# Optimization experiments

Hardware: AMD Instinct MI355X
Metric: run time of the kernel (lower is better)

The kernel has to match this reference:

```python
import jax, jax.numpy as jnp
import numpy as np

B, N, K, D_MODEL = 4, 16384, 32, 64

def gather_neighbors(x, idx):
    # x: [B, N, F], idx: [B, N, K] -> [B, N, K, F]
    return jnp.take_along_axis(x[:, :, None, :], idx[:, :, :, None], axis=1)

def setup_inputs() -> dict:
    key = jax.random.key(0)
    k1, k2, k3, k4, k5 = jax.random.split(key, 5)
    x = jax.random.normal(k1, (B, N, D_MODEL), dtype=jnp.float32)
    pos = jax.random.normal(k2, (B, N, 3), dtype=jnp.float32)
    neighbor_idx = jax.random.randint(k3, (B, N, K), 0, N, dtype=jnp.int32)
    W1 = jax.random.normal(k4, (3, D_MODEL), dtype=jnp.float32) * (1.0 / np.sqrt(3.0))
    b1 = jnp.zeros((D_MODEL,), dtype=jnp.float32)
    W2 = jax.random.normal(k5, (D_MODEL, D_MODEL), dtype=jnp.float32) * (1.0 / np.sqrt(D_MODEL))
    b2 = jnp.zeros((D_MODEL,), dtype=jnp.float32)
    return {"x": x, "pos": pos, "neighbor_idx": neighbor_idx,
            "W1": W1, "b1": b1, "W2": W2, "b2": b2}

def reference(x, pos, neighbor_idx, W1, b1, W2, b2):
    # gather neighbor positions: [B, N, K, 3]
    neighbors = gather_neighbors(pos, neighbor_idx)
    rel_pos = pos[:, :, None, :] - neighbors              # [B, N, K, 3]
    # weight MLP: Linear(3,d) + LeakyReLU(0.1), Linear(d,d)
    h = jax.nn.leaky_relu(jnp.einsum('bnkd,df->bnkf', rel_pos, W1) + b1, 0.1)
    w = jnp.einsum('bnkf,fg->bnkg', h, W2) + b2           # [B, N, K, F]
    xg = gather_neighbors(x, neighbor_idx)                # [B, N, K, F]
    return jnp.sum(w * xg, axis=2)                        # [B, N, F]
```

## Files before the change

### kernel.cpp

```cpp
#include <hip/hip_runtime.h>


#define NPTS   16384
#define KNB    32
#define F      64
#define BATCH  4
#define LOG2N  14
#define WPTS   8

typedef _Float16 h2     __attribute__((ext_vector_type(2)));
typedef _Float16 h8     __attribute__((ext_vector_type(8)));
typedef float    f32x16 __attribute__((ext_vector_type(16)));

__global__ __launch_bounds__(256, 2) void pointconv_mfma(
    const float* __restrict__ x,
    const float* __restrict__ pos,
    const int*   __restrict__ idx,
    const float* __restrict__ W1,
    const float* __restrict__ b1,
    const float* __restrict__ W2,
    const float* __restrict__ b2,
    float*       __restrict__ out)
{
    __shared__ __align__(16) _Float16 w1p[32][8];
    __shared__ __align__(16) _Float16 w2f[2][4][2][32][8];

    const int tid = threadIdx.x;
    if (tid < 32) {
        const int g = 2 * tid;
        w1p[tid][0] = (_Float16)W1[0 * F + g]; w1p[tid][1] = (_Float16)W1[0 * F + g + 1];
        w1p[tid][2] = (_Float16)W1[1 * F + g]; w1p[tid][3] = (_Float16)W1[1 * F + g + 1];
        w1p[tid][4] = (_Float16)W1[2 * F + g]; w1p[tid][5] = (_Float16)W1[2 * F + g + 1];
        w1p[tid][6] = (_Float16)b1[g];         w1p[tid][7] = (_Float16)b1[g + 1];
    }
#pragma unroll
    for (int r = 0; r < 16; ++r) {
        const int e = r * 256 + tid;
        const int g = e >> 6, f = e & 63;
        w2f[(g >> 3) & 1][g >> 4][f & 1][f >> 1][g & 7] = (_Float16)W2[e];
    }
    __syncthreads();

    const int lane = tid & 63;
    const int wv   = tid >> 6;
    const int m    = lane & 31;
    const int hf   = lane >> 5;

    h8 bfrag[4][2];
#pragma unroll
    for (int t = 0; t < 4; ++t)
#pragma unroll
        for (int c = 0; c < 2; ++c)
            bfrag[t][c] = *(const h8*)&w2f[hf][t][c][m][0];

    const float2 b2v = *(const float2*)(b2 + 2 * m);

    const int p0   = (blockIdx.x * 4 + wv) * WPTS;
    const int p0_s = __builtin_amdgcn_readfirstlane(p0);
    const int base = (p0_s >> LOG2N) << LOG2N;
    const float* __restrict__ xb2 = x + (size_t)base * F + 2 * m;

    float rx, ry, rz;
    {
        const int jm = idx[p0_s * KNB + m];
        const int nr = base + jm;
        rx = pos[p0_s * 3 + 0] - pos[nr * 3 + 0];
        ry = pos[p0_s * 3 + 1] - pos[nr * 3 + 1];
        rz = pos[p0_s * 3 + 2] - pos[nr * 3 + 2];
    }

    const h2 c01 = { (_Float16)0.1f, (_Float16)0.1f };

#pragma unroll 1
    for (int i = 0; i < WPTS; ++i) {
        const int p_s = p0_s + i;
        const int* __restrict__ rowp = idx + (size_t)p_s * KNB;

        float2 xv[16];
#pragma unroll
        for (int reg = 0; reg < 16; ++reg) {
            const int rA  = (reg & 3) + ((reg >> 2) << 3);
            const int jlo = rowp[rA];
            const int jhi = rowp[rA + 4];
            const int jk  = hf ? jhi : jlo;
            xv[reg] = *(const float2*)(xb2 + (size_t)jk * F);
        }

        float rxn = 0.f, ryn = 0.f, rzn = 0.f;
        if (i + 1 < WPTS) {
            const int jmn = idx[(p_s + 1) * KNB + m];
            const int nr  = base + jmn;
            rxn = pos[(p_s + 1) * 3 + 0] - pos[nr * 3 + 0];
            ryn = pos[(p_s + 1) * 3 + 1] - pos[nr * 3 + 1];
            rzn = pos[(p_s + 1) * 3 + 2] - pos[nr * 3 + 2];
        }

        f32x16 acc0, acc1;
#pragma unroll
        for (int r = 0; r < 16; ++r) { acc0[r] = b2v.x; acc1[r] = b2v.y; }

        const h2 rxp = { (_Float16)rx, (_Float16)rx };
        const h2 ryp = { (_Float16)ry, (_Float16)ry };
        const h2 rzp = { (_Float16)rz, (_Float16)rz };

#pragma unroll
        for (int t = 0; t < 4; ++t) {
            h8 af;
#pragma unroll
            for (int jj = 0; jj < 4; ++jj) {
                const int g2 = 8 * t + 4 * hf + jj;
                const h8 w = *(const h8*)&w1p[g2][0];
                const h2 wx = __builtin_shufflevector(w, w, 0, 1);
                const h2 wy = __builtin_shufflevector(w, w, 2, 3);
                const h2 wz = __builtin_shufflevector(w, w, 4, 5);
                const h2 bb = __builtin_shufflevector(w, w, 6, 7);
                h2 hv = bb + rxp * wx;
                hv = hv + ryp * wy;
                hv = hv + rzp * wz;
                hv = __builtin_elementwise_max(hv, hv * c01);
                af[2 * jj]     = hv[0];
                af[2 * jj + 1] = hv[1];
            }
            acc0 = __builtin_amdgcn_mfma_f32_32x32x16_f16(af, bfrag[t][0], acc0, 0, 0, 0);
            acc1 = __builtin_amdgcn_mfma_f32_32x32x16_f16(af, bfrag[t][1], acc1, 0, 0, 0);
        }

        float s0 = 0.f, s1 = 0.f;
#pragma unroll
        for (int reg = 0; reg < 16; ++reg) {
            s0 = fmaf(acc0[reg], xv[reg].x, s0);
            s1 = fmaf(acc1[reg], xv[reg].y, s1);
        }
        s0 += __shfl_xor(s0, 32);
        s1 += __shfl_xor(s1, 32);
        if (hf == 0)
            *(float2*)(out + (size_t)p_s * F + 2 * m) = make_float2(s0, s1);

        rx = rxn; ry = ryn; rz = rzn;
    }
}

extern "C" void kernel_launch(void* const* d_in, const int* in_sizes, int n_in,
                              void* d_out, int out_size, void* d_ws, size_t ws_size,
                              hipStream_t stream) {
    const float* x   = (const float*)d_in[0];
    const float* pos = (const float*)d_in[1];
    const int*   idx = (const int*)  d_in[2];
    const float* W1  = (const float*)d_in[3];
    const float* b1  = (const float*)d_in[4];
    const float* W2  = (const float*)d_in[5];
    const float* b2  = (const float*)d_in[6];
    float* out = (float*)d_out;

    dim3 grid((BATCH * NPTS) / (4 * WPTS));
    dim3 block(256);
    pointconv_mfma<<<grid, block, 0, stream>>>(x, pos, idx, W1, b1, W2, b2, out);
}
```

Before: 145.0 us.

## Prefetch next point's neighbor indices into registers and raise occupancy bound

Neighbor indices for the current point are kept in a 32-entry register array, and the next point's row is loaded one iteration early so the x gathers no longer wait on the index loads. The next-point position prefetch loses its branch and clamps to the last point instead. Launch bounds rise from 2 to 3 blocks per CU, which tightens the register budget at the same time the index arrays add register pressure, so spills are a risk.

Measured after the change: 379.1 us. 161% more time.

```diff
diff --git a/kernel.cpp b/kernel.cpp
--- a/kernel.cpp
+++ b/kernel.cpp
@@ -12,7 +12,7 @@
 typedef _Float16 h8     __attribute__((ext_vector_type(8)));
 typedef float    f32x16 __attribute__((ext_vector_type(16)));
 
-__global__ __launch_bounds__(256, 2) void pointconv_mfma(
+__global__ __launch_bounds__(256, 3) void pointconv_mfma(
     const float* __restrict__ x,
     const float* __restrict__ pos,
     const int*   __restrict__ idx,
@@ -60,6 +60,13 @@
     const int base = (p0_s >> LOG2N) << LOG2N;
     const float* __restrict__ xb2 = x + (size_t)base * F + 2 * m;
 
+    int jsc[KNB];
+    {
+        const int* __restrict__ rowp = idx + (size_t)p0_s * KNB;
+#pragma unroll
+        for (int c = 0; c < KNB; ++c) jsc[c] = rowp[c];
+    }
+
     float rx, ry, rz;
     {
         const int jm = idx[p0_s * KNB + m];
@@ -74,25 +81,30 @@
 #pragma unroll 1
     for (int i = 0; i < WPTS; ++i) {
         const int p_s = p0_s + i;
-        const int* __restrict__ rowp = idx + (size_t)p_s * KNB;
+        const int p_n = (i + 1 < WPTS) ? p_s + 1 : p_s;
 
         float2 xv[16];
 #pragma unroll
         for (int reg = 0; reg < 16; ++reg) {
             const int rA  = (reg & 3) + ((reg >> 2) << 3);
-            const int jlo = rowp[rA];
-            const int jhi = rowp[rA + 4];
-            const int jk  = hf ? jhi : jlo;
+            const int jk  = hf ? jsc[rA + 4] : jsc[rA];
             xv[reg] = *(const float2*)(xb2 + (size_t)jk * F);
         }
 
-        float rxn = 0.f, ryn = 0.f, rzn = 0.f;
-        if (i + 1 < WPTS) {
-            const int jmn = idx[(p_s + 1) * KNB + m];
+        int jsn[KNB];
+        {
+            const int* __restrict__ rowp = idx + (size_t)p_n * KNB;
+#pragma unroll
+            for (int c = 0; c < KNB; ++c) jsn[c] = rowp[c];
+        }
+
+        float rxn, ryn, rzn;
+        {
+            const int jmn = idx[(size_t)p_n * KNB + m];
             const int nr  = base + jmn;
-            rxn = pos[(p_s + 1) * 3 + 0] - pos[nr * 3 + 0];
-            ryn = pos[(p_s + 1) * 3 + 1] - pos[nr * 3 + 1];
-            rzn = pos[(p_s + 1) * 3 + 2] - pos[nr * 3 + 2];
+            rxn = pos[p_n * 3 + 0] - pos[nr * 3 + 0];
+            ryn = pos[p_n * 3 + 1] - pos[nr * 3 + 1];
+            rzn = pos[p_n * 3 + 2] - pos[nr * 3 + 2];
         }
 
         f32x16 acc0, acc1;
@@ -136,6 +148,8 @@
         if (hf == 0)
             *(float2*)(out + (size_t)p_s * F + 2 * m) = make_float2(s0, s1);
 
+#pragma unroll
+        for (int c = 0; c < KNB; ++c) jsc[c] = jsn[c];
         rx = rxn; ry = ryn; rz = rzn;
     }
 }
```
